# Kernel tuning notes

Measured on AMD Instinct MI355X. Metric: run time of the kernel, lower is better.

Reference implementation:

```python
import jax, jax.numpy as jnp
import numpy as np
from jax import lax

B, S, E, H = 8, 1024, 1024, 16
HEAD_DIM = E // H
THRESHOLD = 0.5
NEG_FILL = -1e9


def setup_inputs() -> dict:
    key = jax.random.key(0)
    k0, k1, k2 = jax.random.split(key, 3)
    x = jax.random.normal(k0, (B, S, E), jnp.float32)
    in_proj_w = jax.random.normal(k1, (3 * E, E), jnp.float32) * 0.02
    in_proj_b = jnp.zeros((3 * E,), jnp.float32)
    out_proj_w = jax.random.normal(k2, (E, E), jnp.float32) * 0.02
    out_proj_b = jnp.zeros((E,), jnp.float32)
    return {"x": x, "in_proj_w": in_proj_w, "in_proj_b": in_proj_b,
            "out_proj_w": out_proj_w, "out_proj_b": out_proj_b}


def _mha(x, in_proj_w, in_proj_b, out_proj_w, out_proj_b):
    # PyTorch nn.MultiheadAttention with q=k=v=x, batch_first=True
    qkv = x @ in_proj_w.T + in_proj_b                     # [B,S,3E]
    q, k, v = jnp.split(qkv, 3, axis=-1)                  # each [B,S,E]
    def split_heads(t):
        return t.reshape(B, S, H, HEAD_DIM).transpose(0, 2, 1, 3)  # [B,H,S,d]
    q, k, v = split_heads(q), split_heads(k), split_heads(v)
    scale = 1.0 / np.sqrt(HEAD_DIM).astype(np.float32)
    scores = jnp.einsum('bhqd,bhkd->bhqk', q, k) * scale  # [B,H,S,S]
    w = jax.nn.softmax(scores, axis=-1)
    o = jnp.einsum('bhqk,bhkd->bhqd', w, v)               # [B,H,S,d]
    o = o.transpose(0, 2, 1, 3).reshape(B, S, E)
    attn_output = o @ out_proj_w.T + out_proj_b           # [B,S,E]
    attn_weights = w.mean(axis=1)                         # head-averaged [B,S,S]
    return attn_output, attn_weights


def _cluster(attn_weights):
    # Sequential greedy clustering: scan rows i in order; if row i is not yet
    # visited, its high-attention columns (> THRESHOLD) form cluster i and are
    # marked visited. cluster_id[b, j] = row index of the first cluster that
    # claimed token j, or -1 if never claimed.
    visited0 = jnp.zeros((B, S), dtype=bool)
    cid0 = jnp.full((B, S), -1, dtype=jnp.int32)

    def step(carry, i):
        visited, cid = carry
        process = ~jnp.take(visited, i, axis=1)           # [B] row i unvisited?
        high = jnp.take(attn_weights, i, axis=1) > THRESHOLD  # [B,S]
        claimed = process[:, None] & high                 # [B,S]
        newly = claimed & (~visited)
        cid = jnp.where(newly, jnp.int32(i), cid)
        visited = visited | claimed
        return (visited, cid), None

    (visited, cid), _ = lax.scan(step, (visited0, cid0), jnp.arange(S))
    return cid, visited


def reference(x, in_proj_w, in_proj_b, out_proj_w, out_proj_b):
    attn_output, attn_weights = _mha(x, in_proj_w, in_proj_b, out_proj_w, out_proj_b)
    cluster_ids, covered = _cluster(attn_weights)
    # _generate_image_features: x where token belongs to some cluster, -1e9 else
    clustered_outputs = jnp.where(covered[..., None], x, jnp.float32(NEG_FILL))
    return attn_output, attn_weights, clustered_outputs, cluster_ids
```

## Files before the change

### kernel.cpp

```cpp
#include <hip/hip_runtime.h>
#include <hip/hip_bf16.h>

#define B 8
#define S 1024
#define E 1024
#define H 16

typedef unsigned short u16;
typedef unsigned char u8;
typedef unsigned int u32;
typedef unsigned long long u64;

typedef __attribute__((ext_vector_type(8))) short s16x8;
typedef __attribute__((ext_vector_type(4))) float f32x4;
typedef __attribute__((ext_vector_type(16))) float f32x16;

__device__ __forceinline__ u16 f2bf(float f) {
    union { float f; u32 i; } x; x.f = f;
    u32 r = x.i + 0x7FFFu + ((x.i >> 16) & 1u);
    return (u16)(r >> 16);
}
__device__ __forceinline__ f32x16 zero16() {
    f32x16 z;
#pragma unroll
    for (int i = 0; i < 16; ++i) z[i] = 0.f;
    return z;
}
__device__ __forceinline__ void gload16(const u16* g, u16* l) {
    __builtin_amdgcn_global_load_lds(
        (const __attribute__((address_space(1))) u32*)g,
        (__attribute__((address_space(3))) u32*)l, 16, 0, 0);
}

__global__ __launch_bounds__(256) void cvt_all(
    const float* __restrict__ x, const float* __restrict__ w0,
    const float* __restrict__ w1, u16* __restrict__ xb,
    u16* __restrict__ wb0, u16* __restrict__ wb1) {
    int i = blockIdx.x * 256 + threadIdx.x;
    const float* src;
    u16* dst;
    int off;
    if (i < 2097152) { src = x; dst = xb; off = i; }
    else if (i < 2883584) { src = w0; dst = wb0; off = i - 2097152; }
    else { src = w1; dst = wb1; off = i - 2883584; }
    float4 v = ((const float4*)src)[off];
    union { u16 u[4]; ushort4 s; } p;
    p.u[0] = f2bf(v.x); p.u[1] = f2bf(v.y);
    p.u[2] = f2bf(v.z); p.u[3] = f2bf(v.w);
    ((ushort4*)dst)[off] = p.s;
}

__global__ __launch_bounds__(256) void gemm_qkv(
    const u16* __restrict__ A, const u16* __restrict__ W,
    const float* __restrict__ bias, u16* __restrict__ qb, u16* __restrict__ kb,
    u16* __restrict__ vt) {
    __shared__ __align__(16) u16 smem[16384];
    u16* As = smem;
    u16* Bs = smem + 8192;
    const int t = threadIdx.x;
    const int lane = t & 63;
    const int w = t >> 6;
    const int lin = (int)(blockIdx.y * gridDim.x + blockIdx.x);
    const int xcd = lin & 7;
    const int idx = lin >> 3;
    const int mt = (xcd & 3) * 16 + idx / 12;
    const int nt = (xcd >> 2) * 12 + idx % 12;
    const int m0 = mt * 128;
    const int n0 = nt * 128;
    const int wm = w >> 1, wn = w & 1;
    const int l15 = lane & 15, l4 = lane >> 4;
    const int lr = lane >> 3;
    const int lc = ((lane & 7) ^ lr) * 8;

    f32x4 acc[4][4];
#pragma unroll
    for (int i = 0; i < 4; ++i)
#pragma unroll
        for (int j = 0; j < 4; ++j) acc[i][j] = {0.f, 0.f, 0.f, 0.f};

    for (int k0 = 0; k0 < 1024; k0 += 64) {
        __syncthreads();
#pragma unroll
        for (int jj = 0; jj < 4; ++jj) {
            int j = w * 4 + jj;
            gload16(A + (size_t)(m0 + j * 8 + lr) * 1024 + k0 + lc, As + j * 512);
            gload16(W + (size_t)(n0 + j * 8 + lr) * 1024 + k0 + lc, Bs + j * 512);
        }
        __syncthreads();
#pragma unroll
        for (int ks = 0; ks < 2; ++ks) {
            s16x8 af[4], bf[4];
#pragma unroll
            for (int i = 0; i < 4; ++i) {
                int row = wm * 64 + i * 16 + l15;
                af[i] = *(const s16x8*)((const u8*)As +
                        (((row << 7) + (ks << 6) + (l4 << 4)) ^ ((row & 7) << 4)));
            }
#pragma unroll
            for (int j = 0; j < 4; ++j) {
                int row = wn * 64 + j * 16 + l15;
                bf[j] = *(const s16x8*)((const u8*)Bs +
                        (((row << 7) + (ks << 6) + (l4 << 4)) ^ ((row & 7) << 4)));
            }
#pragma unroll
            for (int i = 0; i < 4; ++i)
#pragma unroll
                for (int j = 0; j < 4; ++j)
                    acc[i][j] = __builtin_amdgcn_mfma_f32_16x16x32_bf16(
                        af[i], bf[j], acc[i][j], 0, 0, 0);
        }
    }

    __syncthreads();
    u16* Cs = smem;
    const int seg = n0 >> 10;
    const int bb = m0 >> 10;
    const int ms = m0 & 1023;
    if (seg < 2) {
        const float sc = (seg == 0) ? 0.18033688011f : 1.0f;
#pragma unroll
        for (int j = 0; j < 4; ++j) {
            int nl = wn * 64 + j * 16 + l15;
            float bn = bias[n0 + nl];
#pragma unroll
            for (int i = 0; i < 4; ++i) {
                int ml = wm * 64 + i * 16 + l4 * 4;
#pragma unroll
                for (int rr = 0; rr < 4; ++rr)
                    Cs[(ml + rr) * 128 + nl] = f2bf((acc[i][j][rr] + bn) * sc);
            }
        }
        __syncthreads();
        u16* dst0 = (seg == 0) ? qb : kb;
#pragma unroll
        for (int it = 0; it < 8; ++it) {
            int flat = it * 256 + t;
            int ml = flat >> 4;
            int g = (flat >> 3) & 1;
            int c8 = flat & 7;
            int hh = ((n0 + g * 64) & 1023) >> 6;
            u16* dst = dst0 + (((size_t)(bb * 16 + hh) * 1024 + ms + ml) << 6) + c8 * 8;
            *(uint4*)dst = *(const uint4*)(Cs + ml * 128 + g * 64 + c8 * 8);
        }
    } else {
#pragma unroll
        for (int j = 0; j < 4; ++j) {
            int nl = wn * 64 + j * 16 + l15;
            float bn = bias[n0 + nl];
            int sz = (nl & 7) << 4;
#pragma unroll
            for (int i = 0; i < 4; ++i) {
                int ml = wm * 64 + i * 16 + l4 * 4;
#pragma unroll
                for (int rr = 0; rr < 4; ++rr) {
                    int bl = (ml + rr) << 1;
                    *(u16*)((u8*)Cs + (nl << 8) + (bl ^ sz)) =
                        f2bf(acc[i][j][rr] + bn);
                }
            }
        }
        __syncthreads();
#pragma unroll
        for (int it = 0; it < 8; ++it) {
            int flat = it * 256 + t;
            int nl = flat >> 4;
            int c = flat & 15;
            int n = n0 + nl;
            int hh = (n & 1023) >> 6;
            int d = n & 63;
            u16* dst = vt + ((size_t)(bb * 16 + hh) * 64 + d) * 1024 + ms + c * 8;
            *(uint4*)dst = *(const uint4*)((u8*)Cs + (nl << 8) +
                                           ((c << 4) ^ ((nl & 7) << 4)));
        }
    }
}

__device__ __forceinline__ void gemm1_body(
    int lin, u16* smem, const u16* __restrict__ A, const u16* __restrict__ W,
    const float* __restrict__ bias, float* __restrict__ outf) {
    u16* As = smem;
    u16* Bs = smem + 8192;
    const int t = threadIdx.x;
    const int lane = t & 63;
    const int w = t >> 6;
    const int xcd = lin & 7;
    const int idx = lin >> 3;
    const int m0 = (xcd * 8 + idx / 8) * 128;
    const int n0 = (idx % 8) * 128;
    const int wm = w >> 1, wn = w & 1;
    const int l15 = lane & 15, l4 = lane >> 4;
    const int lr = lane >> 3;
    const int lc = ((lane & 7) ^ lr) * 8;

    f32x4 acc[4][4];
#pragma unroll
    for (int i = 0; i < 4; ++i)
#pragma unroll
        for (int j = 0; j < 4; ++j) acc[i][j] = {0.f, 0.f, 0.f, 0.f};

    for (int k0 = 0; k0 < 1024; k0 += 64) {
        __syncthreads();
#pragma unroll
        for (int jj = 0; jj < 4; ++jj) {
            int j = w * 4 + jj;
            gload16(A + (size_t)(m0 + j * 8 + lr) * 1024 + k0 + lc, As + j * 512);
            gload16(W + (size_t)(n0 + j * 8 + lr) * 1024 + k0 + lc, Bs + j * 512);
        }
        __syncthreads();
#pragma unroll
        for (int ks = 0; ks < 2; ++ks) {
            s16x8 af[4], bf[4];
#pragma unroll
            for (int i = 0; i < 4; ++i) {
                int row = wm * 64 + i * 16 + l15;
                af[i] = *(const s16x8*)((const u8*)As +
                        (((row << 7) + (ks << 6) + (l4 << 4)) ^ ((row & 7) << 4)));
            }
#pragma unroll
            for (int j = 0; j < 4; ++j) {
                int row = wn * 64 + j * 16 + l15;
                bf[j] = *(const s16x8*)((const u8*)Bs +
                        (((row << 7) + (ks << 6) + (l4 << 4)) ^ ((row & 7) << 4)));
            }
#pragma unroll
            for (int i = 0; i < 4; ++i)
#pragma unroll
                for (int j = 0; j < 4; ++j)
                    acc[i][j] = __builtin_amdgcn_mfma_f32_16x16x32_bf16(
                        af[i], bf[j], acc[i][j], 0, 0, 0);
        }
    }

    __syncthreads();
    float* Csf = (float*)smem;
#pragma unroll
    for (int r = 0; r < 2; ++r) {
        if (wm == r) {
#pragma unroll
            for (int j = 0; j < 4; ++j) {
                int nl = wn * 64 + j * 16 + l15;
                float bn = bias[n0 + nl];
#pragma unroll
                for (int i = 0; i < 4; ++i) {
                    int mlr = i * 16 + l4 * 4;
#pragma unroll
                    for (int rr = 0; rr < 4; ++rr)
                        Csf[(mlr + rr) * 128 + nl] = acc[i][j][rr] + bn;
                }
            }
        }
        __syncthreads();
#pragma unroll
        for (int it = 0; it < 8; ++it) {
            int flat = it * 256 + t;
            int row = flat >> 5;
            int c4 = flat & 31;
            *(float4*)(outf + (size_t)(m0 + r * 64 + row) * 1024 + n0 + c4 * 4) =
                *(const float4*)(Csf + row * 128 + c4 * 4);
        }
        __syncthreads();
    }
}

template <int BASE>
__device__ __forceinline__ s16x8 build_pa(f32x16 e) {
    u32 a, bv, c, d;
    asm("v_cvt_pk_bf16_f32 %0, %1, %2" : "=v"(a) : "v"(e[BASE + 0]), "v"(e[BASE + 1]));
    asm("v_cvt_pk_bf16_f32 %0, %1, %2" : "=v"(bv) : "v"(e[BASE + 2]), "v"(e[BASE + 3]));
    asm("v_cvt_pk_bf16_f32 %0, %1, %2" : "=v"(c) : "v"(e[BASE + 4]), "v"(e[BASE + 5]));
    asm("v_cvt_pk_bf16_f32 %0, %1, %2" : "=v"(d) : "v"(e[BASE + 6]), "v"(e[BASE + 7]));
    asm("v_permlane32_swap_b32 %0, %1" : "+v"(a), "+v"(c));
    asm("v_permlane32_swap_b32 %0, %1" : "+v"(bv), "+v"(d));
    union { u32 w[4]; s16x8 v; } u;
    u.w[0] = a; u.w[1] = bv; u.w[2] = c; u.w[3] = d;
    return u.v;
}
__device__ __forceinline__ float pair_max(float v) {
    float a_ = v, b_ = v;
    asm("v_permlane32_swap_b32 %0, %1" : "+v"(a_), "+v"(b_));
    return fmaxf(a_, b_);
}
__device__ __forceinline__ u32 pair_or(u32 v) {
    u32 a_ = v, b_ = v;
    asm("v_permlane32_swap_b32 %0, %1" : "+v"(a_), "+v"(b_));
    return a_ | b_;
}

__global__ __launch_bounds__(256, 4) void attn_flash(
    const u16* __restrict__ qg, const u16* __restrict__ kg,
    const u16* __restrict__ vtg, u16* __restrict__ og,
    float* __restrict__ stats) {
    __shared__ __align__(16) u16 bufK[2][64 * 64];
    __shared__ __align__(16) u16 bufV[2][64 * 64];
    const int t = threadIdx.x;
    const int lane = t & 63;
    const int w = t >> 6;
    const int task = ((blockIdx.x & 7) << 7) | (blockIdx.x >> 3);
    const int b = task >> 7;
    const int h = (task >> 3) & 15;
    const int qg_ = task & 7;
    const int q = lane & 31;
    const int hi = lane >> 5;
    const int q0 = qg_ * 128 + w * 32;
    const size_t hb = (size_t)(b * 16 + h) << 16;

    const int lr = lane >> 3;
    const int lc = ((lane & 7) ^ lr) * 8;
    const int swz = (q & 7) << 4;

    union { u32 wd[4]; s16x8 v; } onesu;
    onesu.wd[0] = 0x3F803F80u; onesu.wd[1] = 0x3F803F80u;
    onesu.wd[2] = 0x3F803F80u; onesu.wd[3] = 0x3F803F80u;
    const s16x8 ones = onesu.v;

#define STAGE(tt, bb)                                                          \
    do {                                                                       \
        _Pragma("unroll") for (int jj = 0; jj < 2; ++jj) {                     \
            int j = w * 2 + jj;                                                \
            gload16(kg + hb + (size_t)((tt) * 64 + j * 8 + lr) * 64 + lc,      \
                    bufK[bb] + j * 512);                                       \
            gload16(vtg + hb + (size_t)(j * 8 + lr) * 1024 + (tt) * 64 + lc,   \
                    bufV[bb] + j * 512);                                       \
        }                                                                      \
    } while (0)

    s16x8 qf[4];
#pragma unroll
    for (int s = 0; s < 4; ++s)
        qf[s] = *(const s16x8*)(qg + hb + (size_t)(q0 + q) * 64 + s * 16 + hi * 8);

    f32x16 oLo = zero16(), oHi = zero16(), lacc = zero16();
    float m = 0.f;

    STAGE(0, 0);
    __syncthreads();
    int cur = 0;

    for (int tile = 0; tile < 16; ++tile) {
        if (tile < 15) STAGE(tile + 1, cur ^ 1);
        const u16* bK = bufK[cur];
        const u16* bV = bufV[cur];
#pragma unroll
        for (int kk = 0; kk < 64; kk += 32) {
            s16x8 ka[4];
#pragma unroll
            for (int s = 0; s < 4; ++s)
                ka[s] = *(const s16x8*)((const u8*)bK +
                        ((((kk + q) << 7) + (s << 5) + (hi << 4)) ^ swz));
            f32x16 s_;
            const float negm = -m;
#pragma unroll
            for (int i = 0; i < 16; ++i) s_[i] = negm;
#pragma unroll
            for (int s = 0; s < 4; ++s)
                s_ = __builtin_amdgcn_mfma_f32_32x32x16_bf16(ka[s], qf[s], s_, 0, 0, 0);
            float m0 = fmaxf(fmaxf(s_[0], s_[4]), fmaxf(s_[8], s_[12]));
            float m1 = fmaxf(fmaxf(s_[1], s_[5]), fmaxf(s_[9], s_[13]));
            float m2 = fmaxf(fmaxf(s_[2], s_[6]), fmaxf(s_[10], s_[14]));
            float m3 = fmaxf(fmaxf(s_[3], s_[7]), fmaxf(s_[11], s_[15]));
            float padj = pair_max(fmaxf(fmaxf(m0, m1), fmaxf(m2, m3)));
            if (__any(padj > 11.5f)) {
                float delta = fmaxf(padj, 0.f);
                float r = exp2f(-delta);
                m += delta;
                lacc[0] *= r;
                oLo = oLo * r;
                oHi = oHi * r;
#pragma unroll
                for (int i = 0; i < 16; ++i) s_[i] -= delta;
            }
#pragma unroll
            for (int i = 0; i < 16; ++i) s_[i] = exp2f(s_[i]);
            s16x8 p0 = build_pa<0>(s_), p1 = build_pa<8>(s_);
            lacc = __builtin_amdgcn_mfma_f32_32x32x16_bf16(ones, p0, lacc, 0, 0, 0);
            lacc = __builtin_amdgcn_mfma_f32_32x32x16_bf16(ones, p1, lacc, 0, 0, 0);
            s16x8 vLo0 = *(const s16x8*)((const u8*)bV +
                         (((q << 7) + (kk << 1) + (hi << 4)) ^ swz));
            s16x8 vLo1 = *(const s16x8*)((const u8*)bV +
                         (((q << 7) + (kk << 1) + 32 + (hi << 4)) ^ swz));
            s16x8 vHi0 = *(const s16x8*)((const u8*)bV +
                         ((((q + 32) << 7) + (kk << 1) + (hi << 4)) ^ swz));
            s16x8 vHi1 = *(const s16x8*)((const u8*)bV +
                         ((((q + 32) << 7) + (kk << 1) + 32 + (hi << 4)) ^ swz));
            oLo = __builtin_amdgcn_mfma_f32_32x32x16_bf16(vLo0, p0, oLo, 0, 0, 0);
            oLo = __builtin_amdgcn_mfma_f32_32x32x16_bf16(vLo1, p1, oLo, 0, 0, 0);
            oHi = __builtin_amdgcn_mfma_f32_32x32x16_bf16(vHi0, p0, oHi, 0, 0, 0);
            oHi = __builtin_amdgcn_mfma_f32_32x32x16_bf16(vHi1, p1, oHi, 0, 0, 0);
        }
        __syncthreads();
        cur ^= 1;
    }
#undef STAGE
    const float l = lacc[0];
    float inv = 1.0f / l;
    oLo = oLo * inv;
    oHi = oHi * inv;
    u16* orow = og + (size_t)(b * 1024 + q0 + q) * 1024 + h * 64;
#pragma unroll
    for (int rg = 0; rg < 4; ++rg) {
        union { u16 u[4]; u64 v; } pk;
#pragma unroll
        for (int j = 0; j < 4; ++j) pk.u[j] = f2bf(oLo[4 * rg + j]);
        *(u64*)(orow + 8 * rg + 4 * hi) = pk.v;
#pragma unroll
        for (int j = 0; j < 4; ++j) pk.u[j] = f2bf(oHi[4 * rg + j]);
        *(u64*)(orow + 32 + 4 * hi + 8 * rg) = pk.v;
    }
    if (hi == 0)
        stats[(size_t)(b * 16 + h) * 1024 + q0 + q] = m + 4.0f + log2f(l);
}

__device__ __forceinline__ void aw_body(
    int bid, u16* smem, const u16* __restrict__ qg, const u16* __restrict__ kg,
    const float* __restrict__ stats, float* __restrict__ aw,
    u64* __restrict__ maskg) {
    u16* bufK = smem;
    u16* bufQ = smem + 8192;
    const int t = threadIdx.x;
    const int lane = t & 63;
    const int w = t >> 6;
    const int sw = ((bid & 7) << 7) | (bid >> 3);
    const int b = sw >> 7;
    const int ks = (sw >> 3) & 15;
    const int qg_ = sw & 7;
    const int q = lane & 31;
    const int hi = lane >> 5;
    const int q0 = qg_ * 128;
    const int qr = w * 32 + q;
    const int kbase = ks * 64;

    const int lr = lane >> 3;
    const int lc = ((lane & 7) ^ lr) * 8;
    const int swz = (q & 7) << 4;

#define STAGEAW(hh, bb)                                                        \
    do {                                                                       \
        const size_t hbs = (size_t)(b * 16 + (hh)) << 16;                      \
        _Pragma("unroll") for (int jj = 0; jj < 2; ++jj) {                     \
            int j = w * 2 + jj;                                                \
            gload16(kg + hbs + (size_t)(kbase + j * 8 + lr) * 64 + lc,         \
                    bufK + (bb) * 4096 + j * 512);                             \
        }                                                                      \
        _Pragma("unroll") for (int jj = 0; jj < 4; ++jj) {                     \
            int j = w * 4 + jj;                                                \
            gload16(qg + hbs + (size_t)(q0 + j * 8 + lr) * 64 + lc,            \
                    bufQ + (bb) * 8192 + j * 512);                             \
        }                                                                      \
    } while (0)

    f32x16 awA = zero16(), awB = zero16();

    STAGEAW(0, 0);
    __syncthreads();
    int cur = 0;

    for (int h = 0; h < 16; ++h) {
        if (h < 15) STAGEAW(h + 1, cur ^ 1);
        const u16* bK = bufK + cur * 4096;
        const u16* bQ = bufQ + cur * 8192;
        s16x8 qf[4], kA[4], kB[4];
#pragma unroll
        for (int s = 0; s < 4; ++s) {
            qf[s] = *(const s16x8*)((const u8*)bQ +
                    (((qr << 7) + (s << 5) + (hi << 4)) ^ swz));
            kA[s] = *(const s16x8*)((const u8*)bK +
                    (((q << 7) + (s << 5) + (hi << 4)) ^ swz));
            kB[s] = *(const s16x8*)((const u8*)bK +
                    ((((q + 32) << 7) + (s << 5) + (hi << 4)) ^ swz));
        }
        float C = stats[(size_t)(b * 16 + h) * 1024 + q0 + qr];
        f32x16 sA, sB;
        const float negC = -C;
#pragma unroll
        for (int i = 0; i < 16; ++i) { sA[i] = negC; sB[i] = negC; }
#pragma unroll
        for (int s = 0; s < 4; ++s) {
            sA = __builtin_amdgcn_mfma_f32_32x32x16_bf16(kA[s], qf[s], sA, 0, 0, 0);
            sB = __builtin_amdgcn_mfma_f32_32x32x16_bf16(kB[s], qf[s], sB, 0, 0, 0);
        }
#pragma unroll
        for (int i = 0; i < 16; ++i) {
            awA[i] += exp2f(sA[i]);
            awB[i] += exp2f(sB[i]);
        }
        __syncthreads();
        cur ^= 1;
    }
#undef STAGEAW
    float* awrow = aw + (size_t)(b * 1024 + q0 + qr) * 1024 + kbase;
#pragma unroll
    for (int rg = 0; rg < 4; ++rg) {
        *(float4*)(awrow + 8 * rg + 4 * hi) =
            make_float4(awA[4 * rg + 0], awA[4 * rg + 1], awA[4 * rg + 2], awA[4 * rg + 3]);
        *(float4*)(awrow + 32 + 8 * rg + 4 * hi) =
            make_float4(awB[4 * rg + 0], awB[4 * rg + 1], awB[4 * rg + 2], awB[4 * rg + 3]);
    }
    u32 lo = 0, hi32 = 0;
#pragma unroll
    for (int r = 0; r < 16; ++r) {
        int k = (r & 3) + 8 * (r >> 2) + 4 * hi;
        lo |= (awA[r] > 0.5f) ? (1u << k) : 0u;
        hi32 |= (awB[r] > 0.5f) ? (1u << k) : 0u;
    }
    lo = pair_or(lo);
    hi32 = pair_or(hi32);
    if (hi == 0)
        maskg[(size_t)(b * 1024 + q0 + qr) * 16 + ks] = ((u64)hi32 << 32) | (u64)lo;
}

__global__ __launch_bounds__(256, 3) void attn_aw_k(
    const u16* __restrict__ qg, const u16* __restrict__ kg,
    const float* __restrict__ stats, float* __restrict__ aw,
    u64* __restrict__ maskg) {
    __shared__ __align__(16) u16 sm[24576];
    aw_body((int)blockIdx.x, sm, qg, kg, stats, aw, maskg);
}
__global__ __launch_bounds__(256, 3) void gemm1_k(
    const u16* __restrict__ A, const u16* __restrict__ W,
    const float* __restrict__ bias, float* __restrict__ outf) {
    __shared__ __align__(16) u16 sm[16384];
    gemm1_body((int)blockIdx.x, sm, A, W, bias, outf);
}
__global__ __launch_bounds__(256, 3) void fused_aw_gemm1(
    const u16* __restrict__ qg, const u16* __restrict__ kg,
    const float* __restrict__ stats, float* __restrict__ aw,
    u64* __restrict__ maskg, const u16* __restrict__ o,
    const u16* __restrict__ w1, const float* __restrict__ bias,
    float* __restrict__ outf) {
    __shared__ __align__(16) u16 sm[24576];
    if (blockIdx.x < 1024)
        aw_body((int)blockIdx.x, sm, qg, kg, stats, aw, maskg);
    else
        gemm1_body((int)blockIdx.x - 1024, sm, o, w1, bias, outf);
}

__global__ __launch_bounds__(256) void cluster_kernel(
    const u64* __restrict__ maskg, float* __restrict__ cid, u64* __restrict__ cov) {
    __shared__ u64 mask[16384];
    __shared__ u16 rows[1024];
    const int t = threadIdx.x;
    const int b = blockIdx.x;
#pragma unroll
    for (int i = 0; i < 64; ++i)
        mask[t + 256 * i] = maskg[(size_t)b * 16384 + t + 256 * i];
#pragma unroll
    for (int i = 0; i < 4; ++i) cid[b * S + t + 256 * i] = -1.0f;
    __syncthreads();
    if (t < 64) {
        int nr = 0;
        for (int it = 0; it < 16; ++it) {
            int row = it * 64 + t;
            const u64* mp = mask + row * 16;
            u64 orv = 0;
#pragma unroll
            for (int j = 0; j < 16; ++j) orv |= mp[j];
            u64 bal = __ballot(orv != 0ULL);
            int pre = __popcll(bal & ((1ULL << t) - 1ULL));
            if (orv != 0ULL) rows[nr + pre] = (u16)row;
            nr += __popcll(bal);
        }
        u64 vis = 0;
        for (int idx = 0; idx < nr; ++idx) {
            int i = rows[idx];
            u64 viw = __shfl(vis, i >> 6);
            bool proc = ((viw >> (i & 63)) & 1ULL) == 0ULL;
            u64 cl = (proc && t < 16) ? mask[i * 16 + t] : 0ULL;
            u64 newly = cl & ~vis;
            vis |= cl;
            while (newly) {
                int bit = __ffsll((long long)newly) - 1;
                cid[b * S + t * 64 + bit] = (float)i;
                newly &= newly - 1;
            }
        }
        if (t < 16) cov[b * 16 + t] = vis;
    }
}

__global__ __launch_bounds__(256) void clustered_kernel(
    const float* __restrict__ x, const u64* __restrict__ cov,
    float* __restrict__ out2) {
    const size_t n4 = (size_t)B * S * E / 4;
    size_t idx = (size_t)blockIdx.x * 256 + threadIdx.x;
    const float4 neg = make_float4(-1e9f, -1e9f, -1e9f, -1e9f);
    for (; idx < n4; idx += (size_t)gridDim.x * 256) {
        size_t tok = idx >> 8;
        int bb = (int)(tok >> 10), s = (int)(tok & 1023);
        u64 m = cov[bb * 16 + (s >> 6)];
        bool c = ((m >> (s & 63)) & 1ULL) != 0ULL;
        float4 v = ((const float4*)x)[idx];
        ((float4*)out2)[idx] = c ? v : neg;
    }
}

extern "C" void kernel_launch(void* const* d_in, const int* in_sizes, int n_in,
                              void* d_out, int out_size, void* d_ws, size_t ws_size,
                              hipStream_t stream) {
    const float* x = (const float*)d_in[0];
    const float* w_in = (const float*)d_in[1];
    const float* b_in = (const float*)d_in[2];
    const float* w_out = (const float*)d_in[3];
    const float* b_out = (const float*)d_in[4];

    float* out0 = (float*)d_out;
    float* out1 = out0 + 8388608;
    float* out2 = out1 + 8388608;
    float* out3 = out2 + 8388608;

    if (ws_size >= ((size_t)37 << 20)) {
        u16* o_bf = (u16*)d_ws;
        u16* q_bf = (u16*)((char*)d_ws + ((size_t)16 << 20));
        u16* wb1 = (u16*)((char*)d_ws + ((size_t)32 << 20));
        float* statsF = (float*)((char*)d_ws + ((size_t)34 << 20));
        u64* maskg = (u64*)((char*)d_ws + ((size_t)34 << 20) + (1u << 19));
        u64* cov = (u64*)((char*)d_ws + ((size_t)35 << 20) + (1u << 19));
        u16* vt_bf = (u16*)out0;
        u16* xb = (u16*)out1;
        u16* wb0 = xb + 8388608;
        u16* k_bf = (u16*)out2;

        cvt_all<<<12288, 256, 0, stream>>>(x, w_in, w_out, xb, wb0, wb1);
        gemm_qkv<<<dim3(64, 24), 256, 0, stream>>>(xb, wb0, b_in, q_bf, k_bf, vt_bf);
        attn_flash<<<1024, 256, 0, stream>>>(q_bf, k_bf, vt_bf, o_bf, statsF);
        fused_aw_gemm1<<<1536, 256, 0, stream>>>(q_bf, k_bf, statsF, out1, maskg,
                                                 o_bf, wb1, b_out, out0);
        cluster_kernel<<<8, 256, 0, stream>>>(maskg, out3, cov);
        clustered_kernel<<<2048, 256, 0, stream>>>(x, cov, out2);
    } else {
        u16* q_bf = (u16*)out0;
        u16* vt_bf = q_bf + 8388608;
        u16* xb = (u16*)out1;
        u16* k_bf = (u16*)out2;
        u16* wb0 = k_bf + 8388608;
        u16* wb1 = wb0 + 3145728;
        float* statsF = (float*)(k_bf + 12582912);
        u16* o_bf = (u16*)d_ws;
        u64* maskg = (u64*)((char*)d_ws + (size_t)(16u << 20));
        u64* cov = (u64*)((char*)d_ws + (size_t)(17u << 20));

        cvt_all<<<12288, 256, 0, stream>>>(x, w_in, w_out, xb, wb0, wb1);
        gemm_qkv<<<dim3(64, 24), 256, 0, stream>>>(xb, wb0, b_in, q_bf, k_bf, vt_bf);
        attn_flash<<<1024, 256, 0, stream>>>(q_bf, k_bf, vt_bf, o_bf, statsF);
        attn_aw_k<<<1024, 256, 0, stream>>>(q_bf, k_bf, statsF, out1, maskg);
        gemm1_k<<<512, 256, 0, stream>>>(o_bf, wb1, b_out, out0);
        cluster_kernel<<<8, 256, 0, stream>>>(maskg, out3, cov);
        clustered_kernel<<<2048, 256, 0, stream>>>(x, cov, out2);
    }
}
```

Before: 239.7 us.

## Process full 64-key tile per step and replace MFMA row-sum with VALU sum

The flash-attention inner loop now computes scores for both 32-key halves of a tile at once, so there is one max/rescale check per 64 keys instead of two. The softmax denominator is built with scalar adds and a lane-pair swap sum rather than two extra MFMAs against a ones vector. Launch bounds drop from 4 to 3 waves per SIMD to give room for the extra score registers. This removes MFMA work and halves rescale checks, at the cost of more VALU adds, higher register pressure and lower occupancy.

```diff
diff --git a/kernel.cpp b/kernel.cpp
--- a/kernel.cpp
+++ b/kernel.cpp
@@ -280,13 +280,18 @@
     asm("v_permlane32_swap_b32 %0, %1" : "+v"(a_), "+v"(b_));
     return fmaxf(a_, b_);
 }
+__device__ __forceinline__ float pair_sum(float v) {
+    float a_ = v, b_ = v;
+    asm("v_permlane32_swap_b32 %0, %1" : "+v"(a_), "+v"(b_));
+    return a_ + b_;
+}
 __device__ __forceinline__ u32 pair_or(u32 v) {
     u32 a_ = v, b_ = v;
     asm("v_permlane32_swap_b32 %0, %1" : "+v"(a_), "+v"(b_));
     return a_ | b_;
 }
 
-__global__ __launch_bounds__(256, 4) void attn_flash(
+__global__ __launch_bounds__(256, 3) void attn_flash(
     const u16* __restrict__ qg, const u16* __restrict__ kg,
     const u16* __restrict__ vtg, u16* __restrict__ og,
     float* __restrict__ stats) {
@@ -308,11 +313,6 @@
     const int lc = ((lane & 7) ^ lr) * 8;
     const int swz = (q & 7) << 4;
 
-    union { u32 wd[4]; s16x8 v; } onesu;
-    onesu.wd[0] = 0x3F803F80u; onesu.wd[1] = 0x3F803F80u;
-    onesu.wd[2] = 0x3F803F80u; onesu.wd[3] = 0x3F803F80u;
-    const s16x8 ones = onesu.v;
-
 #define STAGE(tt, bb)                                                          \
     do {                                                                       \
         _Pragma("unroll") for (int jj = 0; jj < 2; ++jj) {                     \
@@ -329,8 +329,8 @@
     for (int s = 0; s < 4; ++s)
         qf[s] = *(const s16x8*)(qg + hb + (size_t)(q0 + q) * 64 + s * 16 + hi * 8);
 
-    f32x16 oLo = zero16(), oHi = zero16(), lacc = zero16();
-    float m = 0.f;
+    f32x16 oLo = zero16(), oHi = zero16();
+    float m = 0.f, l = 0.f;
 
     STAGE(0, 0);
     __syncthreads();
@@ -340,58 +340,75 @@
         if (tile < 15) STAGE(tile + 1, cur ^ 1);
         const u16* bK = bufK[cur];
         const u16* bV = bufV[cur];
-#pragma unroll
-        for (int kk = 0; kk < 64; kk += 32) {
-            s16x8 ka[4];
-#pragma unroll
-            for (int s = 0; s < 4; ++s)
-                ka[s] = *(const s16x8*)((const u8*)bK +
-                        ((((kk + q) << 7) + (s << 5) + (hi << 4)) ^ swz));
-            f32x16 s_;
-            const float negm = -m;
-#pragma unroll
-            for (int i = 0; i < 16; ++i) s_[i] = negm;
-#pragma unroll
-            for (int s = 0; s < 4; ++s)
-                s_ = __builtin_amdgcn_mfma_f32_32x32x16_bf16(ka[s], qf[s], s_, 0, 0, 0);
-            float m0 = fmaxf(fmaxf(s_[0], s_[4]), fmaxf(s_[8], s_[12]));
-            float m1 = fmaxf(fmaxf(s_[1], s_[5]), fmaxf(s_[9], s_[13]));
-            float m2 = fmaxf(fmaxf(s_[2], s_[6]), fmaxf(s_[10], s_[14]));
-            float m3 = fmaxf(fmaxf(s_[3], s_[7]), fmaxf(s_[11], s_[15]));
-            float padj = pair_max(fmaxf(fmaxf(m0, m1), fmaxf(m2, m3)));
-            if (__any(padj > 11.5f)) {
-                float delta = fmaxf(padj, 0.f);
-                float r = exp2f(-delta);
-                m += delta;
-                lacc[0] *= r;
-                oLo = oLo * r;
-                oHi = oHi * r;
-#pragma unroll
-                for (int i = 0; i < 16; ++i) s_[i] -= delta;
-            }
-#pragma unroll
-            for (int i = 0; i < 16; ++i) s_[i] = exp2f(s_[i]);
-            s16x8 p0 = build_pa<0>(s_), p1 = build_pa<8>(s_);
-            lacc = __builtin_amdgcn_mfma_f32_32x32x16_bf16(ones, p0, lacc, 0, 0, 0);
-            lacc = __builtin_amdgcn_mfma_f32_32x32x16_bf16(ones, p1, lacc, 0, 0, 0);
-            s16x8 vLo0 = *(const s16x8*)((const u8*)bV +
-                         (((q << 7) + (kk << 1) + (hi << 4)) ^ swz));
-            s16x8 vLo1 = *(const s16x8*)((const u8*)bV +
-                         (((q << 7) + (kk << 1) + 32 + (hi << 4)) ^ swz));
-            s16x8 vHi0 = *(const s16x8*)((const u8*)bV +
-                         ((((q + 32) << 7) + (kk << 1) + (hi << 4)) ^ swz));
-            s16x8 vHi1 = *(const s16x8*)((const u8*)bV +
-                         ((((q + 32) << 7) + (kk << 1) + 32 + (hi << 4)) ^ swz));
-            oLo = __builtin_amdgcn_mfma_f32_32x32x16_bf16(vLo0, p0, oLo, 0, 0, 0);
-            oLo = __builtin_amdgcn_mfma_f32_32x32x16_bf16(vLo1, p1, oLo, 0, 0, 0);
-            oHi = __builtin_amdgcn_mfma_f32_32x32x16_bf16(vHi0, p0, oHi, 0, 0, 0);
-            oHi = __builtin_amdgcn_mfma_f32_32x32x16_bf16(vHi1, p1, oHi, 0, 0, 0);
-        }
+        s16x8 ka0[4], ka1[4];
+#pragma unroll
+        for (int s = 0; s < 4; ++s) {
+            ka0[s] = *(const s16x8*)((const u8*)bK +
+                     (((q << 7) + (s << 5) + (hi << 4)) ^ swz));
+            ka1[s] = *(const s16x8*)((const u8*)bK +
+                     ((((32 + q) << 7) + (s << 5) + (hi << 4)) ^ swz));
+        }
+        f32x16 s0_, s1_;
+        const float negm = -m;
+#pragma unroll
+        for (int i = 0; i < 16; ++i) { s0_[i] = negm; s1_[i] = negm; }
+#pragma unroll
+        for (int s = 0; s < 4; ++s) {
+            s0_ = __builtin_amdgcn_mfma_f32_32x32x16_bf16(ka0[s], qf[s], s0_, 0, 0, 0);
+            s1_ = __builtin_amdgcn_mfma_f32_32x32x16_bf16(ka1[s], qf[s], s1_, 0, 0, 0);
+        }
+        float m0 = fmaxf(fmaxf(s0_[0], s0_[4]), fmaxf(s0_[8], s0_[12]));
+        float m1 = fmaxf(fmaxf(s0_[1], s0_[5]), fmaxf(s0_[9], s0_[13]));
+        float m2 = fmaxf(fmaxf(s0_[2], s0_[6]), fmaxf(s0_[10], s0_[14]));
+        float m3 = fmaxf(fmaxf(s0_[3], s0_[7]), fmaxf(s0_[11], s0_[15]));
+        m0 = fmaxf(m0, fmaxf(fmaxf(s1_[0], s1_[4]), fmaxf(s1_[8], s1_[12])));
+        m1 = fmaxf(m1, fmaxf(fmaxf(s1_[1], s1_[5]), fmaxf(s1_[9], s1_[13])));
+        m2 = fmaxf(m2, fmaxf(fmaxf(s1_[2], s1_[6]), fmaxf(s1_[10], s1_[14])));
+        m3 = fmaxf(m3, fmaxf(fmaxf(s1_[3], s1_[7]), fmaxf(s1_[11], s1_[15])));
+        float padj = pair_max(fmaxf(fmaxf(m0, m1), fmaxf(m2, m3)));
+        if (__any(padj > 11.5f)) {
+            float delta = fmaxf(padj, 0.f);
+            float r = exp2f(-delta);
+            m += delta;
+            l *= r;
+            oLo = oLo * r;
+            oHi = oHi * r;
+#pragma unroll
+            for (int i = 0; i < 16; ++i) { s0_[i] -= delta; s1_[i] -= delta; }
+        }
+        float t0 = 0.f, t1 = 0.f, t2 = 0.f, t3 = 0.f;
+#pragma unroll
+        for (int i = 0; i < 16; i += 4) {
+            s0_[i + 0] = exp2f(s0_[i + 0]); s1_[i + 0] = exp2f(s1_[i + 0]);
+            s0_[i + 1] = exp2f(s0_[i + 1]); s1_[i + 1] = exp2f(s1_[i + 1]);
+            s0_[i + 2] = exp2f(s0_[i + 2]); s1_[i + 2] = exp2f(s1_[i + 2]);
+            s0_[i + 3] = exp2f(s0_[i + 3]); s1_[i + 3] = exp2f(s1_[i + 3]);
+            t0 += s0_[i + 0] + s1_[i + 0]; t1 += s0_[i + 1] + s1_[i + 1];
+            t2 += s0_[i + 2] + s1_[i + 2]; t3 += s0_[i + 3] + s1_[i + 3];
+        }
+        l += pair_sum((t0 + t1) + (t2 + t3));
+        s16x8 p00 = build_pa<0>(s0_), p01 = build_pa<8>(s0_);
+        s16x8 p10 = build_pa<0>(s1_), p11 = build_pa<8>(s1_);
+        s16x8 vA = *(const s16x8*)((const u8*)bV + (((q << 7) + 0 + (hi << 4)) ^ swz));
+        s16x8 vB = *(const s16x8*)((const u8*)bV + ((((q + 32) << 7) + 0 + (hi << 4)) ^ swz));
+        oLo = __builtin_amdgcn_mfma_f32_32x32x16_bf16(vA, p00, oLo, 0, 0, 0);
+        oHi = __builtin_amdgcn_mfma_f32_32x32x16_bf16(vB, p00, oHi, 0, 0, 0);
+        vA = *(const s16x8*)((const u8*)bV + (((q << 7) + 32 + (hi << 4)) ^ swz));
+        vB = *(const s16x8*)((const u8*)bV + ((((q + 32) << 7) + 32 + (hi << 4)) ^ swz));
+        oLo = __builtin_amdgcn_mfma_f32_32x32x16_bf16(vA, p01, oLo, 0, 0, 0);
+        oHi = __builtin_amdgcn_mfma_f32_32x32x16_bf16(vB, p01, oHi, 0, 0, 0);
+        vA = *(const s16x8*)((const u8*)bV + (((q << 7) + 64 + (hi << 4)) ^ swz));
+        vB = *(const s16x8*)((const u8*)bV + ((((q + 32) << 7) + 64 + (hi << 4)) ^ swz));
+        oLo = __builtin_amdgcn_mfma_f32_32x32x16_bf16(vA, p10, oLo, 0, 0, 0);
+        oHi = __builtin_amdgcn_mfma_f32_32x32x16_bf16(vB, p10, oHi, 0, 0, 0);
+        vA = *(const s16x8*)((const u8*)bV + (((q << 7) + 96 + (hi << 4)) ^ swz));
+        vB = *(const s16x8*)((const u8*)bV + ((((q + 32) << 7) + 96 + (hi << 4)) ^ swz));
+        oLo = __builtin_amdgcn_mfma_f32_32x32x16_bf16(vA, p11, oLo, 0, 0, 0);
+        oHi = __builtin_amdgcn_mfma_f32_32x32x16_bf16(vB, p11, oHi, 0, 0, 0);
         __syncthreads();
         cur ^= 1;
     }
 #undef STAGE
-    const float l = lacc[0];
     float inv = 1.0f / l;
     oLo = oLo * inv;
     oHi = oHi * inv;
```

Result: faster. 230.2 us (-4.0%).

## Shrink flash-attention blocks to two waves, sum softmax denominator on VALU, add MFMA priority

Applied to the files above, without the earlier changes.

The flash attention kernel now runs 2048 blocks of 128 threads (64 query rows each) instead of 1024 blocks of 256, and each wave stages twice as many K/V rows per tile. The row-sum of exponentials is now accumulated with scalar adds plus a cross-half permlane swap, replacing the two extra MFMAs against a ones matrix. s_setprio brackets are added around the MFMA groups. The aim is finer block granularity and less matrix-unit work per tile. The cost is that K/V tiles are reused by fewer waves, so LDS and global staging traffic per query rises.

```diff
diff --git a/kernel.cpp b/kernel.cpp
--- a/kernel.cpp
+++ b/kernel.cpp
@@ -280,13 +280,18 @@
     asm("v_permlane32_swap_b32 %0, %1" : "+v"(a_), "+v"(b_));
     return fmaxf(a_, b_);
 }
+__device__ __forceinline__ float pair_sum(float v) {
+    float a_ = v, b_ = v;
+    asm("v_permlane32_swap_b32 %0, %1" : "+v"(a_), "+v"(b_));
+    return a_ + b_;
+}
 __device__ __forceinline__ u32 pair_or(u32 v) {
     u32 a_ = v, b_ = v;
     asm("v_permlane32_swap_b32 %0, %1" : "+v"(a_), "+v"(b_));
     return a_ | b_;
 }
 
-__global__ __launch_bounds__(256, 4) void attn_flash(
+__global__ __launch_bounds__(128, 3) void attn_flash(
     const u16* __restrict__ qg, const u16* __restrict__ kg,
     const u16* __restrict__ vtg, u16* __restrict__ og,
     float* __restrict__ stats) {
@@ -295,28 +300,23 @@
     const int t = threadIdx.x;
     const int lane = t & 63;
     const int w = t >> 6;
-    const int task = ((blockIdx.x & 7) << 7) | (blockIdx.x >> 3);
-    const int b = task >> 7;
-    const int h = (task >> 3) & 15;
-    const int qg_ = task & 7;
+    const int task = ((blockIdx.x & 7) << 8) | (blockIdx.x >> 3);
+    const int b = task >> 8;
+    const int h = (task >> 4) & 15;
+    const int qg_ = task & 15;
     const int q = lane & 31;
     const int hi = lane >> 5;
-    const int q0 = qg_ * 128 + w * 32;
+    const int q0 = qg_ * 64 + w * 32;
     const size_t hb = (size_t)(b * 16 + h) << 16;
 
     const int lr = lane >> 3;
     const int lc = ((lane & 7) ^ lr) * 8;
     const int swz = (q & 7) << 4;
 
-    union { u32 wd[4]; s16x8 v; } onesu;
-    onesu.wd[0] = 0x3F803F80u; onesu.wd[1] = 0x3F803F80u;
-    onesu.wd[2] = 0x3F803F80u; onesu.wd[3] = 0x3F803F80u;
-    const s16x8 ones = onesu.v;
-
 #define STAGE(tt, bb)                                                          \
     do {                                                                       \
-        _Pragma("unroll") for (int jj = 0; jj < 2; ++jj) {                     \
-            int j = w * 2 + jj;                                                \
+        _Pragma("unroll") for (int jj = 0; jj < 4; ++jj) {                     \
+            int j = w * 4 + jj;                                                \
             gload16(kg + hb + (size_t)((tt) * 64 + j * 8 + lr) * 64 + lc,      \
                     bufK[bb] + j * 512);                                       \
             gload16(vtg + hb + (size_t)(j * 8 + lr) * 1024 + (tt) * 64 + lc,   \
@@ -329,8 +329,8 @@
     for (int s = 0; s < 4; ++s)
         qf[s] = *(const s16x8*)(qg + hb + (size_t)(q0 + q) * 64 + s * 16 + hi * 8);
 
-    f32x16 oLo = zero16(), oHi = zero16(), lacc = zero16();
-    float m = 0.f;
+    f32x16 oLo = zero16(), oHi = zero16();
+    float m = 0.f, l = 0.f;
 
     STAGE(0, 0);
     __syncthreads();
@@ -351,9 +351,11 @@
             const float negm = -m;
 #pragma unroll
             for (int i = 0; i < 16; ++i) s_[i] = negm;
+            __builtin_amdgcn_s_setprio(1);
 #pragma unroll
             for (int s = 0; s < 4; ++s)
                 s_ = __builtin_amdgcn_mfma_f32_32x32x16_bf16(ka[s], qf[s], s_, 0, 0, 0);
+            __builtin_amdgcn_s_setprio(0);
             float m0 = fmaxf(fmaxf(s_[0], s_[4]), fmaxf(s_[8], s_[12]));
             float m1 = fmaxf(fmaxf(s_[1], s_[5]), fmaxf(s_[9], s_[13]));
             float m2 = fmaxf(fmaxf(s_[2], s_[6]), fmaxf(s_[10], s_[14]));
@@ -363,17 +365,23 @@
                 float delta = fmaxf(padj, 0.f);
                 float r = exp2f(-delta);
                 m += delta;
-                lacc[0] *= r;
+                l *= r;
                 oLo = oLo * r;
                 oHi = oHi * r;
 #pragma unroll
                 for (int i = 0; i < 16; ++i) s_[i] -= delta;
             }
-#pragma unroll
-            for (int i = 0; i < 16; ++i) s_[i] = exp2f(s_[i]);
+            float t0 = 0.f, t1 = 0.f, t2 = 0.f, t3 = 0.f;
+#pragma unroll
+            for (int i = 0; i < 16; i += 4) {
+                s_[i + 0] = exp2f(s_[i + 0]);
+                s_[i + 1] = exp2f(s_[i + 1]);
+                s_[i + 2] = exp2f(s_[i + 2]);
+                s_[i + 3] = exp2f(s_[i + 3]);
+                t0 += s_[i + 0]; t1 += s_[i + 1]; t2 += s_[i + 2]; t3 += s_[i + 3];
+            }
+            l += pair_sum((t0 + t1) + (t2 + t3));
             s16x8 p0 = build_pa<0>(s_), p1 = build_pa<8>(s_);
-            lacc = __builtin_amdgcn_mfma_f32_32x32x16_bf16(ones, p0, lacc, 0, 0, 0);
-            lacc = __builtin_amdgcn_mfma_f32_32x32x16_bf16(ones, p1, lacc, 0, 0, 0);
             s16x8 vLo0 = *(const s16x8*)((const u8*)bV +
                          (((q << 7) + (kk << 1) + (hi << 4)) ^ swz));
             s16x8 vLo1 = *(const s16x8*)((const u8*)bV +
@@ -382,16 +390,17 @@
                          ((((q + 32) << 7) + (kk << 1) + (hi << 4)) ^ swz));
             s16x8 vHi1 = *(const s16x8*)((const u8*)bV +
                          ((((q + 32) << 7) + (kk << 1) + 32 + (hi << 4)) ^ swz));
+            __builtin_amdgcn_s_setprio(1);
             oLo = __builtin_amdgcn_mfma_f32_32x32x16_bf16(vLo0, p0, oLo, 0, 0, 0);
             oLo = __builtin_amdgcn_mfma_f32_32x32x16_bf16(vLo1, p1, oLo, 0, 0, 0);
             oHi = __builtin_amdgcn_mfma_f32_32x32x16_bf16(vHi0, p0, oHi, 0, 0, 0);
             oHi = __builtin_amdgcn_mfma_f32_32x32x16_bf16(vHi1, p1, oHi, 0, 0, 0);
+            __builtin_amdgcn_s_setprio(0);
         }
         __syncthreads();
         cur ^= 1;
     }
 #undef STAGE
-    const float l = lacc[0];
     float inv = 1.0f / l;
     oLo = oLo * inv;
     oHi = oHi * inv;
@@ -621,7 +630,7 @@
 
         cvt_all<<<12288, 256, 0, stream>>>(x, w_in, w_out, xb, wb0, wb1);
         gemm_qkv<<<dim3(64, 24), 256, 0, stream>>>(xb, wb0, b_in, q_bf, k_bf, vt_bf);
-        attn_flash<<<1024, 256, 0, stream>>>(q_bf, k_bf, vt_bf, o_bf, statsF);
+        attn_flash<<<2048, 128, 0, stream>>>(q_bf, k_bf, vt_bf, o_bf, statsF);
         fused_aw_gemm1<<<1536, 256, 0, stream>>>(q_bf, k_bf, statsF, out1, maskg,
                                                  o_bf, wb1, b_out, out0);
         cluster_kernel<<<8, 256, 0, stream>>>(maskg, out3, cov);
@@ -640,7 +649,7 @@
 
         cvt_all<<<12288, 256, 0, stream>>>(x, w_in, w_out, xb, wb0, wb1);
         gemm_qkv<<<dim3(64, 24), 256, 0, stream>>>(xb, wb0, b_in, q_bf, k_bf, vt_bf);
-        attn_flash<<<1024, 256, 0, stream>>>(q_bf, k_bf, vt_bf, o_bf, statsF);
+        attn_flash<<<2048, 128, 0, stream>>>(q_bf, k_bf, vt_bf, o_bf, statsF);
         attn_aw_k<<<1024, 256, 0, stream>>>(q_bf, k_bf, statsF, out1, maskg);
         gemm1_k<<<512, 256, 0, stream>>>(o_bf, wb1, b_out, out0);
         cluster_kernel<<<8, 256, 0, stream>>>(maskg, out3, cov);
```

After: 256.3 us. +6.9%, slower.
